# Kernel optimization log

Hardware: AMD Instinct MI355X
Metric: run time of the kernel (lower is better)

The kernel has to match this reference:

```python
import jax, jax.numpy as jnp
import numpy as np

NUM_HEADS = 12  # from init_kwargs


def setup_inputs() -> dict:
    key = jax.random.key(0)
    k1, k2, k3 = jax.random.split(key, 3)
    B, N, C = 8, 4096, 768
    x = jax.random.normal(k1, (B, N, C), dtype=jnp.float32)
    qkv_w = jax.random.normal(k2, (3 * C, C), dtype=jnp.float32) * (C ** -0.5)
    proj_w = jax.random.normal(k3, (C, C), dtype=jnp.float32) * (C ** -0.5)
    proj_b = jnp.zeros((C,), dtype=jnp.float32)
    return {"x": x, "qkv_w": qkv_w, "proj_w": proj_w, "proj_b": proj_b}


def reference(x, qkv_w, proj_w, proj_b):
    B, N, C = x.shape
    H = NUM_HEADS
    hd = C // H
    h = w = int(round(N ** 0.5))  # spatial grid, N = h*w
    # fused qkv projection (q, k are produced but never consumed, as in source)
    qkv = jnp.einsum('bnc,dc->bnd', x, qkv_w)          # [B, N, 3C]
    qkv = qkv.reshape(B, N, 3, H, hd)
    v = qkv[:, :, 2].transpose(0, 2, 1, 3)             # [B, H, N, hd]
    v2d = v.reshape(B, H, h, w, hd)
    # fft2 over spatial dims; concat(real, imag) then slice[:hd] == real part
    v_real = jnp.fft.fft2(v2d.astype(jnp.float32), axes=(2, 3)).real
    out = v_real.reshape(B, H, N, hd).transpose(0, 2, 1, 3).reshape(B, N, C)
    return jnp.einsum('bnc,dc->bnd', out, proj_w) + proj_b
```

## Files before the change

kernel.cpp:

```cpp
#include <hip/hip_runtime.h>
#include <hip/hip_bf16.h>


typedef __bf16 bf16x8 __attribute__((ext_vector_type(8)));
typedef __bf16 bf16x4 __attribute__((ext_vector_type(4)));
typedef float f32x4 __attribute__((ext_vector_type(4)));
typedef float f32x16 __attribute__((ext_vector_type(16)));
typedef unsigned short ushort_t;
typedef unsigned int uint_t;

typedef __attribute__((address_space(3))) unsigned int lds_u32;
typedef __attribute__((address_space(1))) unsigned int glob_u32;

__device__ __forceinline__ void gl_lds16(const void* g, void* l) {
  __builtin_amdgcn_global_load_lds((const glob_u32*)g, (lds_u32*)l, 16, 0, 0);
}

__device__ __forceinline__ ushort_t f2bf(float f) {
  union { __hip_bfloat16 h; ushort_t s; } cv;
  cv.h = __float2bfloat16(f);
  return cv.s;
}

__device__ __forceinline__ bf16x8 ld_frag(const ushort_t* p) {
  union { bf16x8 v; bf16x4 h[2]; } r;
  r.h[0] = *(const bf16x4*)p;
  r.h[1] = *(const bf16x4*)(p + 4);
  return r.v;
}

__device__ __forceinline__ bf16x8 tw_frag(int m, int k0, bool use_sin, float sign) {
  union { bf16x8 v; ushort_t u[8]; } r;
#pragma unroll
  for (int j = 0; j < 8; ++j) {
    int ph = (m * (k0 + j)) & 63;
    float a = (float)ph * 0.09817477042468104f;
    float x = use_sin ? __sinf(a) : __cosf(a);
    r.u[j] = f2bf(sign * x);
  }
  return r.v;
}

__global__ __launch_bounds__(256) void fft_a_pre(const float* __restrict__ X,
                                                 const float* __restrict__ P,
                                                 const float* __restrict__ Q,
                                                 __hip_bfloat16* __restrict__ Ar,
                                                 __hip_bfloat16* __restrict__ Ai,
                                                 __hip_bfloat16* __restrict__ Mb) {
  __shared__ ushort_t smem[9728];
  const int t = threadIdx.x;
  const int c0 = blockIdx.x * 128;
  const int w = t >> 6, l = t & 63;
  const int lm = l & 15, lq = l >> 4;

  if (blockIdx.y < 512) {
    ushort_t* Xs = smem;
    ushort_t* Ep = smem;
    const int s = blockIdx.y;
    const float* src = X + (size_t)s * 64 * 768 + c0;
#pragma unroll
    for (int it = 0; it < 16; ++it) {
      int p = it * 256 + t;
      int c = p & 127, pr = p >> 7;
      float a = src[(size_t)(2 * pr) * 768 + c];
      float b = src[(size_t)(2 * pr + 1) * 768 + c];
      union { ushort_t u[2]; uint_t w_; } pk;
      pk.u[0] = f2bf(a); pk.u[1] = f2bf(b);
      *(uint_t*)&Xs[c * 68 + 2 * pr] = pk.w_;
    }
    __syncthreads();
    bf16x8 afc[3][2], afs[3][2];
#pragma unroll
    for (int mt = 0; mt < 3; ++mt)
#pragma unroll
      for (int ks = 0; ks < 2; ++ks) {
        int m = mt * 16 + lm;
        int k0 = ks * 32 + lq * 8;
        afc[mt][ks] = tw_frag(m, k0, false, 1.f);
        afs[mt][ks] = tw_frag(m, k0, true, 1.f);
      }
    f32x4 accr[3][2] = {}, acci[3][2] = {};
#pragma unroll
    for (int ks = 0; ks < 2; ++ks) {
      bf16x8 bf[2];
#pragma unroll
      for (int nt = 0; nt < 2; ++nt) {
        int c = w * 32 + nt * 16 + lm;
        bf[nt] = ld_frag(&Xs[c * 68 + ks * 32 + lq * 8]);
      }
#pragma unroll
      for (int mt = 0; mt < 3; ++mt)
#pragma unroll
        for (int nt = 0; nt < 2; ++nt) {
          accr[mt][nt] = __builtin_amdgcn_mfma_f32_16x16x32_bf16(afc[mt][ks], bf[nt], accr[mt][nt], 0, 0, 0);
          acci[mt][nt] = __builtin_amdgcn_mfma_f32_16x16x32_bf16(afs[mt][ks], bf[nt], acci[mt][nt], 0, 0, 0);
        }
    }
#pragma unroll
    for (int arr = 0; arr < 2; ++arr) {
      __syncthreads();
#pragma unroll
      for (int mt = 0; mt < 3; ++mt)
#pragma unroll
        for (int nt = 0; nt < 2; ++nt)
#pragma unroll
          for (int r = 0; r < 4; ++r) {
            int row = mt * 16 + lq * 4 + r;
            int col = w * 32 + nt * 16 + lm;
            float v = arr ? acci[mt][nt][r] : accr[mt][nt][r];
            Ep[row * 136 + col] = f2bf(v);
          }
      __syncthreads();
      __hip_bfloat16* dst = arr ? Ai : Ar;
#pragma unroll
      for (int it = 0; it < 3; ++it) {
        int idx = it * 256 + t;
        int row = idx >> 4, cq = (idx & 15) * 8;
        if (row <= 32) {
          uint4 v = *(const uint4*)&Ep[row * 136 + cq];
          *(uint4*)&dst[(size_t)(s * 64 + row) * 768 + c0 + cq] = v;
        }
      }
    }
  } else {
    ushort_t* As = smem;
    ushort_t* Bs = smem + 5120;
    const int i0 = (blockIdx.y - 512) * 128;
    const int wm = w & 1, wn = w >> 1;
    f32x4 acc[4][4] = {};
    for (int kt = 0; kt < 24; ++kt) {
      const int k0 = kt * 32;
      {
        int e = t * 16, row = e >> 5, dc = e & 16;
        const float* src = &P[(size_t)(i0 + row) * 768 + k0 + dc];
        float4 f0 = *(const float4*)&src[0], f1 = *(const float4*)&src[4];
        float4 f2 = *(const float4*)&src[8], f3 = *(const float4*)&src[12];
        union { ushort_t u[8]; uint4 v; } pk0, pk1;
        pk0.u[0] = f2bf(f0.x); pk0.u[1] = f2bf(f0.y); pk0.u[2] = f2bf(f0.z); pk0.u[3] = f2bf(f0.w);
        pk0.u[4] = f2bf(f1.x); pk0.u[5] = f2bf(f1.y); pk0.u[6] = f2bf(f1.z); pk0.u[7] = f2bf(f1.w);
        pk1.u[0] = f2bf(f2.x); pk1.u[1] = f2bf(f2.y); pk1.u[2] = f2bf(f2.z); pk1.u[3] = f2bf(f2.w);
        pk1.u[4] = f2bf(f3.x); pk1.u[5] = f2bf(f3.y); pk1.u[6] = f2bf(f3.z); pk1.u[7] = f2bf(f3.w);
        *(uint4*)&As[row * 40 + dc] = pk0.v;
        *(uint4*)&As[row * 40 + dc + 8] = pk1.v;
      }
#pragma unroll
      for (int it = 0; it < 8; ++it) {
        int p = it * 256 + t, c = p & 127, pr = p >> 7;
        float a = Q[(size_t)(1536 + k0 + 2 * pr) * 768 + c0 + c];
        float b = Q[(size_t)(1536 + k0 + 2 * pr + 1) * 768 + c0 + c];
        union { ushort_t u[2]; uint_t w_; } pk;
        pk.u[0] = f2bf(a); pk.u[1] = f2bf(b);
        *(uint_t*)&Bs[c * 36 + 2 * pr] = pk.w_;
      }
      __syncthreads();
      bf16x8 af[4], bfr[4];
#pragma unroll
      for (int mt = 0; mt < 4; ++mt)
        af[mt] = ld_frag(&As[(wm * 64 + mt * 16 + lm) * 40 + lq * 8]);
#pragma unroll
      for (int nt = 0; nt < 4; ++nt)
        bfr[nt] = ld_frag(&Bs[(wn * 64 + nt * 16 + lm) * 36 + lq * 8]);
#pragma unroll
      for (int mt = 0; mt < 4; ++mt)
#pragma unroll
        for (int nt = 0; nt < 4; ++nt)
          acc[mt][nt] = __builtin_amdgcn_mfma_f32_16x16x32_bf16(af[mt], bfr[nt], acc[mt][nt], 0, 0, 0);
      __syncthreads();
    }
#pragma unroll
    for (int nt = 0; nt < 4; ++nt) {
      const int col = c0 + wn * 64 + nt * 16 + lm;
#pragma unroll
      for (int mt = 0; mt < 4; ++mt) {
        const int rbase = i0 + wm * 64 + mt * 16 + lq * 4;
#pragma unroll
        for (int r = 0; r < 4; ++r)
          Mb[(size_t)(rbase + r) * 768 + col] = __float2bfloat16(acc[mt][nt][r]);
      }
    }
  }
}

__global__ __launch_bounds__(256) void fft_b_mfma(const __hip_bfloat16* __restrict__ Ar,
                                                  const __hip_bfloat16* __restrict__ Ai,
                                                  __hip_bfloat16* __restrict__ Xf) {
  __shared__ ushort_t smem[17408];
  ushort_t* Rs = smem;
  ushort_t* Is = smem + 8704;
  ushort_t* Ep = smem;
  const int t = threadIdx.x;
  const int bz = blockIdx.y;
  const int b = bz / 33, k2 = bz % 33;
  const int c0 = blockIdx.x * 128;
  const ushort_t* ar = (const ushort_t*)Ar + ((size_t)(b * 64) * 64 + k2) * 768 + c0;
  const ushort_t* ai = (const ushort_t*)Ai + ((size_t)(b * 64) * 64 + k2) * 768 + c0;
  const size_t n1s = (size_t)64 * 768;
#pragma unroll
  for (int it = 0; it < 16; ++it) {
    int p = it * 256 + t;
    int c = p & 127, pr = p >> 7;
    size_t o0 = (size_t)(2 * pr) * n1s + c;
    size_t o1 = o0 + n1s;
    union { ushort_t u[2]; uint_t w_; } p1, p2;
    p1.u[0] = ar[o0]; p1.u[1] = ar[o1];
    p2.u[0] = ai[o0]; p2.u[1] = ai[o1];
    *(uint_t*)&Rs[c * 68 + 2 * pr] = p1.w_;
    *(uint_t*)&Is[c * 68 + 2 * pr] = p2.w_;
  }
  __syncthreads();
  const int w = t >> 6, l = t & 63;
  const int wm = w & 1, wn = w >> 1;
  const int lm = l & 15, lq = l >> 4;
  bf16x8 afc[2][2], afs[2][2];
#pragma unroll
  for (int mt = 0; mt < 2; ++mt)
#pragma unroll
    for (int ks = 0; ks < 2; ++ks) {
      int m = wm * 32 + mt * 16 + lm;
      int k0 = ks * 32 + lq * 8;
      afc[mt][ks] = tw_frag(m, k0, false, 1.f);
      afs[mt][ks] = tw_frag(m, k0, true, 1.f);
    }
  f32x4 accC[2][4] = {}, accS[2][4] = {};
#pragma unroll
  for (int ks = 0; ks < 2; ++ks) {
    bf16x8 bR[4], bI[4];
#pragma unroll
    for (int nt = 0; nt < 4; ++nt) {
      int c = wn * 64 + nt * 16 + lm;
      int kb = ks * 32 + lq * 8;
      bR[nt] = ld_frag(&Rs[c * 68 + kb]);
      bI[nt] = ld_frag(&Is[c * 68 + kb]);
    }
#pragma unroll
    for (int mt = 0; mt < 2; ++mt)
#pragma unroll
      for (int nt = 0; nt < 4; ++nt) {
        accC[mt][nt] = __builtin_amdgcn_mfma_f32_16x16x32_bf16(afc[mt][ks], bR[nt], accC[mt][nt], 0, 0, 0);
        accS[mt][nt] = __builtin_amdgcn_mfma_f32_16x16x32_bf16(afs[mt][ks], bI[nt], accS[mt][nt], 0, 0, 0);
      }
  }
  const int nout = (k2 >= 1 && k2 <= 31) ? 2 : 1;
  for (int o = 0; o < nout; ++o) {
    __syncthreads();
#pragma unroll
    for (int mt = 0; mt < 2; ++mt)
#pragma unroll
      for (int nt = 0; nt < 4; ++nt)
#pragma unroll
        for (int r = 0; r < 4; ++r) {
          int row = wm * 32 + mt * 16 + lq * 4 + r;
          int col = wn * 64 + nt * 16 + lm;
          float v = o ? (accC[mt][nt][r] + accS[mt][nt][r])
                      : (accC[mt][nt][r] - accS[mt][nt][r]);
          Ep[row * 136 + col] = f2bf(v);
        }
    __syncthreads();
    const int k2o = o ? (64 - k2) : k2;
#pragma unroll
    for (int it = 0; it < 4; ++it) {
      int idx = it * 256 + t;
      int k1 = idx >> 4, cq = (idx & 15) * 8;
      uint4 v = *(const uint4*)&Ep[k1 * 136 + cq];
      *(uint4*)&Xf[((size_t)b * 4096 + k1 * 64 + k2o) * 768 + c0 + cq] = v;
    }
  }
}

__global__ __launch_bounds__(256) void gemm_bt(const __hip_bfloat16* __restrict__ A,
                                               const __hip_bfloat16* __restrict__ B,
                                               const float* __restrict__ bias,
                                               float* __restrict__ C) {
  __shared__ ushort_t As[128 * 64];
  __shared__ ushort_t Bs[128 * 64];
  const int t = threadIdx.x, w = t >> 6, l = t & 63;
  const int L = blockIdx.x + blockIdx.y * 6;
  const int s = L >> 3, xcd = L & 7;
  const int n0 = (s % 6) * 128;
  const int m0 = ((s / 6) * 8 + xcd) * 128;
  const int wm = w & 1, wn = w >> 1;
  f32x16 acc[2][2] = {};
  const int srow = l >> 3;
  const int schunk = (l & 7) ^ srow;
  const int lr = l & 31, lh = l >> 5;
  for (int kt = 0; kt < 12; ++kt) {
    const int k0 = kt * 64;
#pragma unroll
    for (int i = 0; i < 4; ++i) {
      const int rbase = w * 32 + i * 8;
      const int row = rbase + srow;
      gl_lds16(&A[(size_t)(m0 + row) * 768 + k0 + schunk * 8], &As[rbase * 64]);
      gl_lds16(&B[(size_t)(n0 + row) * 768 + k0 + schunk * 8], &Bs[rbase * 64]);
    }
    __syncthreads();
#pragma unroll
    for (int ks = 0; ks < 4; ++ks) {
      bf16x8 af[2], bf[2];
#pragma unroll
      for (int mt = 0; mt < 2; ++mt) {
        int row = wm * 64 + mt * 32 + lr;
        int ch = (ks * 2 + lh) ^ (lr & 7);
        af[mt] = *(const bf16x8*)&As[row * 64 + ch * 8];
      }
#pragma unroll
      for (int nt = 0; nt < 2; ++nt) {
        int row = wn * 64 + nt * 32 + lr;
        int ch = (ks * 2 + lh) ^ (lr & 7);
        bf[nt] = *(const bf16x8*)&Bs[row * 64 + ch * 8];
      }
#pragma unroll
      for (int mt = 0; mt < 2; ++mt)
#pragma unroll
        for (int nt = 0; nt < 2; ++nt)
          acc[mt][nt] = __builtin_amdgcn_mfma_f32_32x32x16_bf16(af[mt], bf[nt], acc[mt][nt], 0, 0, 0);
    }
    __syncthreads();
  }
#pragma unroll
  for (int nt = 0; nt < 2; ++nt) {
    const int col = n0 + wn * 64 + nt * 32 + lr;
    const float bv = bias[col];
#pragma unroll
    for (int mt = 0; mt < 2; ++mt) {
      const int rb = m0 + wm * 64 + mt * 32 + 4 * lh;
#pragma unroll
      for (int reg = 0; reg < 16; ++reg) {
        const int row = rb + (reg & 3) + 8 * (reg >> 2);
        C[(size_t)row * 768 + col] = acc[mt][nt][reg] + bv;
      }
    }
  }
}

extern "C" void kernel_launch(void* const* d_in, const int* in_sizes, int n_in,
                              void* d_out, int out_size, void* d_ws, size_t ws_size,
                              hipStream_t stream) {
  const float* x      = (const float*)d_in[0];
  const float* qkv_w  = (const float*)d_in[1];
  const float* proj_w = (const float*)d_in[2];
  const float* proj_b = (const float*)d_in[3];
  float* out = (float*)d_out;

  char* ws = (char*)d_ws;
  const size_t MB_BYTES = (size_t)768 * 768 * 2;
  const size_t ARR_BYTES = (size_t)8 * 4096 * 768 * 2;
  __hip_bfloat16* Mb = (__hip_bfloat16*)ws;
  __hip_bfloat16* Ar = (__hip_bfloat16*)(ws + MB_BYTES);
  __hip_bfloat16* Ai = (__hip_bfloat16*)(ws + MB_BYTES + ARR_BYTES);
  __hip_bfloat16* Xf = (__hip_bfloat16*)(ws + MB_BYTES + 2 * ARR_BYTES);

  fft_a_pre<<<dim3(6, 518), 256, 0, stream>>>(x, proj_w, qkv_w, Ar, Ai, Mb);
  fft_b_mfma<<<dim3(6, 264), 256, 0, stream>>>(Ar, Ai, Xf);
  gemm_bt<<<dim3(6, 256), 256, 0, stream>>>(Xf, Mb, proj_b, out);
}
```

Before: 282.4 us.

## Precompute twiddle fragments in a table and vectorize global-to-LDS transpose loads

```diff
diff --git a/kernel.cpp b/kernel.cpp
--- a/kernel.cpp
+++ b/kernel.cpp
@@ -29,16 +29,33 @@
   return r.v;
 }
 
-__device__ __forceinline__ bf16x8 tw_frag(int m, int k0, bool use_sin, float sign) {
-  union { bf16x8 v; ushort_t u[8]; } r;
-#pragma unroll
-  for (int j = 0; j < 8; ++j) {
-    int ph = (m * (k0 + j)) & 63;
+__global__ __launch_bounds__(256) void tw_init(ushort_t* __restrict__ TwA,
+                                               ushort_t* __restrict__ TwB) {
+  const int id = blockIdx.x * 256 + threadIdx.x;
+  int m, k0, sn;
+  ushort_t* out;
+  if (id < 768) {
+    int r = id % 384, cs = id / 384;
+    int l = r & 63, ks = (r >> 6) & 1, mt = r >> 7;
+    m = mt * 16 + (l & 15);
+    k0 = ks * 32 + (l >> 4) * 8;
+    sn = cs;
+    out = TwA + id * 8;
+  } else {
+    int j = id - 768;
+    int r = j % 512, cs = j / 512;
+    int l = r & 63, ks = (r >> 6) & 1, mt = (r >> 7) & 1, wm = r >> 8;
+    m = wm * 32 + mt * 16 + (l & 15);
+    k0 = ks * 32 + (l >> 4) * 8;
+    sn = cs;
+    out = TwB + j * 8;
+  }
+#pragma unroll
+  for (int e = 0; e < 8; ++e) {
+    int ph = (m * (k0 + e)) & 63;
     float a = (float)ph * 0.09817477042468104f;
-    float x = use_sin ? __sinf(a) : __cosf(a);
-    r.u[j] = f2bf(sign * x);
-  }
-  return r.v;
+    out[e] = f2bf(sn ? __sinf(a) : __cosf(a));
+  }
 }
 
 __global__ __launch_bounds__(256) void fft_a_pre(const float* __restrict__ X,
@@ -46,39 +63,42 @@
                                                  const float* __restrict__ Q,
                                                  __hip_bfloat16* __restrict__ Ar,
                                                  __hip_bfloat16* __restrict__ Ai,
-                                                 __hip_bfloat16* __restrict__ Mb) {
+                                                 __hip_bfloat16* __restrict__ Mb,
+                                                 const ushort_t* __restrict__ TwA) {
   __shared__ ushort_t smem[9728];
   const int t = threadIdx.x;
   const int c0 = blockIdx.x * 128;
   const int w = t >> 6, l = t & 63;
   const int lm = l & 15, lq = l >> 4;
 
-  if (blockIdx.y < 512) {
+  if (blockIdx.y >= 6) {
     ushort_t* Xs = smem;
     ushort_t* Ep = smem;
-    const int s = blockIdx.y;
+    const int s = blockIdx.y - 6;
     const float* src = X + (size_t)s * 64 * 768 + c0;
-#pragma unroll
-    for (int it = 0; it < 16; ++it) {
-      int p = it * 256 + t;
-      int c = p & 127, pr = p >> 7;
-      float a = src[(size_t)(2 * pr) * 768 + c];
-      float b = src[(size_t)(2 * pr + 1) * 768 + c];
-      union { ushort_t u[2]; uint_t w_; } pk;
-      pk.u[0] = f2bf(a); pk.u[1] = f2bf(b);
-      *(uint_t*)&Xs[c * 68 + 2 * pr] = pk.w_;
-    }
-    __syncthreads();
+    const bf16x8* twa = (const bf16x8*)TwA;
     bf16x8 afc[3][2], afs[3][2];
 #pragma unroll
     for (int mt = 0; mt < 3; ++mt)
 #pragma unroll
       for (int ks = 0; ks < 2; ++ks) {
-        int m = mt * 16 + lm;
-        int k0 = ks * 32 + lq * 8;
-        afc[mt][ks] = tw_frag(m, k0, false, 1.f);
-        afs[mt][ks] = tw_frag(m, k0, true, 1.f);
-      }
+        afc[mt][ks] = twa[mt * 128 + ks * 64 + l];
+        afs[mt][ks] = twa[384 + mt * 128 + ks * 64 + l];
+      }
+#pragma unroll
+    for (int it = 0; it < 4; ++it) {
+      const int pr = it * 8 + (t >> 5);
+      const int c = (t & 31) * 4;
+      const float* rp = src + (size_t)(2 * pr) * 768 + c;
+      f32x4 f0 = *(const f32x4*)rp;
+      f32x4 f1 = *(const f32x4*)(rp + 768);
+#pragma unroll
+      for (int j = 0; j < 4; ++j) {
+        uint_t pk = (uint_t)f2bf(f0[j]) | ((uint_t)f2bf(f1[j]) << 16);
+        *(uint_t*)&Xs[(c + j) * 68 + 2 * pr] = pk;
+      }
+    }
+    __syncthreads();
     f32x4 accr[3][2] = {}, acci[3][2] = {};
 #pragma unroll
     for (int ks = 0; ks < 2; ++ks) {
@@ -125,7 +145,7 @@
   } else {
     ushort_t* As = smem;
     ushort_t* Bs = smem + 5120;
-    const int i0 = (blockIdx.y - 512) * 128;
+    const int i0 = blockIdx.y * 128;
     const int wm = w & 1, wn = w >> 1;
     f32x4 acc[4][4] = {};
     for (int kt = 0; kt < 24; ++kt) {
@@ -144,13 +164,17 @@
         *(uint4*)&As[row * 40 + dc + 8] = pk1.v;
       }
 #pragma unroll
-      for (int it = 0; it < 8; ++it) {
-        int p = it * 256 + t, c = p & 127, pr = p >> 7;
-        float a = Q[(size_t)(1536 + k0 + 2 * pr) * 768 + c0 + c];
-        float b = Q[(size_t)(1536 + k0 + 2 * pr + 1) * 768 + c0 + c];
-        union { ushort_t u[2]; uint_t w_; } pk;
-        pk.u[0] = f2bf(a); pk.u[1] = f2bf(b);
-        *(uint_t*)&Bs[c * 36 + 2 * pr] = pk.w_;
+      for (int it = 0; it < 2; ++it) {
+        const int pr = it * 8 + (t >> 5);
+        const int c = (t & 31) * 4;
+        const float* qp = Q + (size_t)(1536 + k0 + 2 * pr) * 768 + c0 + c;
+        f32x4 q0 = *(const f32x4*)qp;
+        f32x4 q1 = *(const f32x4*)(qp + 768);
+#pragma unroll
+        for (int j = 0; j < 4; ++j) {
+          uint_t pk = (uint_t)f2bf(q0[j]) | ((uint_t)f2bf(q1[j]) << 16);
+          *(uint_t*)&Bs[(c + j) * 36 + 2 * pr] = pk;
+        }
       }
       __syncthreads();
       bf16x8 af[4], bfr[4];
@@ -183,7 +207,8 @@
 
 __global__ __launch_bounds__(256) void fft_b_mfma(const __hip_bfloat16* __restrict__ Ar,
                                                   const __hip_bfloat16* __restrict__ Ai,
-                                                  __hip_bfloat16* __restrict__ Xf) {
+                                                  __hip_bfloat16* __restrict__ Xf,
+                                                  const ushort_t* __restrict__ TwB) {
   __shared__ ushort_t smem[17408];
   ushort_t* Rs = smem;
   ushort_t* Is = smem + 8704;
@@ -195,32 +220,45 @@
   const ushort_t* ar = (const ushort_t*)Ar + ((size_t)(b * 64) * 64 + k2) * 768 + c0;
   const ushort_t* ai = (const ushort_t*)Ai + ((size_t)(b * 64) * 64 + k2) * 768 + c0;
   const size_t n1s = (size_t)64 * 768;
-#pragma unroll
-  for (int it = 0; it < 16; ++it) {
-    int p = it * 256 + t;
-    int c = p & 127, pr = p >> 7;
-    size_t o0 = (size_t)(2 * pr) * n1s + c;
-    size_t o1 = o0 + n1s;
-    union { ushort_t u[2]; uint_t w_; } p1, p2;
-    p1.u[0] = ar[o0]; p1.u[1] = ar[o1];
-    p2.u[0] = ai[o0]; p2.u[1] = ai[o1];
-    *(uint_t*)&Rs[c * 68 + 2 * pr] = p1.w_;
-    *(uint_t*)&Is[c * 68 + 2 * pr] = p2.w_;
-  }
-  __syncthreads();
   const int w = t >> 6, l = t & 63;
   const int wm = w & 1, wn = w >> 1;
   const int lm = l & 15, lq = l >> 4;
+  const bf16x8* twb = (const bf16x8*)TwB;
   bf16x8 afc[2][2], afs[2][2];
 #pragma unroll
   for (int mt = 0; mt < 2; ++mt)
 #pragma unroll
     for (int ks = 0; ks < 2; ++ks) {
-      int m = wm * 32 + mt * 16 + lm;
-      int k0 = ks * 32 + lq * 8;
-      afc[mt][ks] = tw_frag(m, k0, false, 1.f);
-      afs[mt][ks] = tw_frag(m, k0, true, 1.f);
-    }
+      afc[mt][ks] = twb[wm * 256 + mt * 128 + ks * 64 + l];
+      afs[mt][ks] = twb[512 + wm * 256 + mt * 128 + ks * 64 + l];
+    }
+#pragma unroll
+  for (int it = 0; it < 4; ++it) {
+    const int pr = it * 8 + (t >> 5);
+    const int c = (t & 31) * 4;
+    const size_t o0 = (size_t)(2 * pr) * n1s + c;
+    uint2 va = *(const uint2*)&ar[o0];
+    uint2 vb = *(const uint2*)&ar[o0 + n1s];
+    uint2 ia = *(const uint2*)&ai[o0];
+    uint2 ib = *(const uint2*)&ai[o0 + n1s];
+    uint_t r0 = (va.x & 0xffffu) | (vb.x << 16);
+    uint_t r1 = (va.x >> 16) | (vb.x & 0xffff0000u);
+    uint_t r2 = (va.y & 0xffffu) | (vb.y << 16);
+    uint_t r3 = (va.y >> 16) | (vb.y & 0xffff0000u);
+    *(uint_t*)&Rs[(c + 0) * 68 + 2 * pr] = r0;
+    *(uint_t*)&Rs[(c + 1) * 68 + 2 * pr] = r1;
+    *(uint_t*)&Rs[(c + 2) * 68 + 2 * pr] = r2;
+    *(uint_t*)&Rs[(c + 3) * 68 + 2 * pr] = r3;
+    uint_t s0 = (ia.x & 0xffffu) | (ib.x << 16);
+    uint_t s1 = (ia.x >> 16) | (ib.x & 0xffff0000u);
+    uint_t s2 = (ia.y & 0xffffu) | (ib.y << 16);
+    uint_t s3 = (ia.y >> 16) | (ib.y & 0xffff0000u);
+    *(uint_t*)&Is[(c + 0) * 68 + 2 * pr] = s0;
+    *(uint_t*)&Is[(c + 1) * 68 + 2 * pr] = s1;
+    *(uint_t*)&Is[(c + 2) * 68 + 2 * pr] = s2;
+    *(uint_t*)&Is[(c + 3) * 68 + 2 * pr] = s3;
+  }
+  __syncthreads();
   f32x4 accC[2][4] = {}, accS[2][4] = {};
 #pragma unroll
   for (int ks = 0; ks < 2; ++ks) {
@@ -348,8 +386,11 @@
   __hip_bfloat16* Ar = (__hip_bfloat16*)(ws + MB_BYTES);
   __hip_bfloat16* Ai = (__hip_bfloat16*)(ws + MB_BYTES + ARR_BYTES);
   __hip_bfloat16* Xf = (__hip_bfloat16*)(ws + MB_BYTES + 2 * ARR_BYTES);
-
-  fft_a_pre<<<dim3(6, 518), 256, 0, stream>>>(x, proj_w, qkv_w, Ar, Ai, Mb);
-  fft_b_mfma<<<dim3(6, 264), 256, 0, stream>>>(Ar, Ai, Xf);
+  ushort_t* TwA = (ushort_t*)((char*)Ar + 61440);
+  ushort_t* TwB = (ushort_t*)((char*)Ar + 61440 + 12288);
+
+  tw_init<<<dim3(7), 256, 0, stream>>>(TwA, TwB);
+  fft_a_pre<<<dim3(6, 518), 256, 0, stream>>>(x, proj_w, qkv_w, Ar, Ai, Mb, TwA);
+  fft_b_mfma<<<dim3(6, 264), 256, 0, stream>>>(Ar, Ai, Xf, TwB);
   gemm_bt<<<dim3(6, 256), 256, 0, stream>>>(Xf, Mb, proj_b, out);
 }
```

New measurement: 271.2 us. -4.0%, faster.
